# Kernel tuning notes

Hardware: AMD Instinct MI355X
Metric: run time of the kernel (lower is better)

## Reference

```python
import jax, jax.numpy as jnp
import numpy as np

N_NODES = 100000
N_EDGES = 1600000
D_IN = 128
D_HID = 128
N_CLASSES = 4
N_GRAPHS = 512


def setup_inputs() -> dict:
    key = jax.random.key(0)
    ks = jax.random.split(key, 10)
    x = jax.random.normal(ks[0], (N_NODES, D_IN), dtype=jnp.float32)
    edge_index = jax.random.randint(ks[1], (2, N_EDGES), 0, N_NODES, dtype=jnp.int64)
    batch = jnp.sort(jax.random.randint(ks[2], (N_NODES,), 0, N_GRAPHS, dtype=jnp.int64))
    s = 1.0 / np.sqrt(D_IN)
    W1l = jax.random.uniform(ks[3], (D_HID, D_IN), jnp.float32, -s, s)
    W1r = jax.random.uniform(ks[4], (D_HID, D_IN), jnp.float32, -s, s)
    b1 = jnp.zeros((D_HID,), jnp.float32)
    s2 = 1.0 / np.sqrt(D_HID)
    W2l = jax.random.uniform(ks[5], (D_HID, D_HID), jnp.float32, -s2, s2)
    W2r = jax.random.uniform(ks[6], (D_HID, D_HID), jnp.float32, -s2, s2)
    b2 = jnp.zeros((D_HID,), jnp.float32)
    Wlin = jax.random.uniform(ks[7], (N_CLASSES, D_HID), jnp.float32, -s2, s2)
    blin = jax.random.uniform(ks[8], (N_CLASSES,), jnp.float32, -s2, s2)
    return {"x": x, "edge_index": edge_index, "batch": batch,
            "W1l": W1l, "b1": b1, "W1r": W1r,
            "W2l": W2l, "b2": b2, "W2r": W2r,
            "Wlin": Wlin, "blin": blin}


def _sage_conv(x, src, dst, deg_inv, W_l, b, W_r):
    # mean-aggregate neighbor features (messages flow src -> dst)
    agg = jax.ops.segment_sum(x[src], dst, num_segments=N_NODES) * deg_inv
    return agg @ W_l.T + b + x @ W_r.T


def reference(x, edge_index, batch, W1l, b1, W1r, W2l, b2, W2r, Wlin, blin):
    src, dst = edge_index[0], edge_index[1]
    ones = jnp.ones((src.shape[0],), x.dtype)
    deg = jax.ops.segment_sum(ones, dst, num_segments=N_NODES)
    deg_inv = (1.0 / jnp.maximum(deg, 1.0))[:, None]

    h = jax.nn.relu(_sage_conv(x, src, dst, deg_inv, W1l, b1, W1r))
    h = jax.nn.relu(_sage_conv(h, src, dst, deg_inv, W2l, b2, W2r))

    # global mean pool over graphs
    gsum = jax.ops.segment_sum(h, batch, num_segments=N_GRAPHS)
    gcnt = jax.ops.segment_sum(jnp.ones((N_NODES,), h.dtype), batch, num_segments=N_GRAPHS)
    pooled = gsum / jnp.maximum(gcnt, 1.0)[:, None]

    # dropout is identity in eval mode
    return pooled @ Wlin.T + blin
```

## Files before the change

kernel.cpp:

```cpp
#include <hip/hip_runtime.h>
#include <hip/hip_bf16.h>


#define NN 100000
#define NE 1600000
#define DH 128
#define NG 512
#define CSTRIDE 48
#define NPREP 6250

#define SUBSH 8
#define SUBN  256
#define NSUB  391
#define CAP   4608
#define NSCAN 256
#define ESPS  6250

#define PSUM_SCALE  1048576.0f
#define PSUM_INV    (1.0f/1048576.0f)

typedef __hip_bfloat16 bf16;
typedef __bf16 bf16x8 __attribute__((ext_vector_type(8)));
typedef float  f32x4  __attribute__((ext_vector_type(4)));
typedef float  f32x2  __attribute__((ext_vector_type(2)));
typedef unsigned u32x2 __attribute__((ext_vector_type(2)));
typedef unsigned u32x4 __attribute__((ext_vector_type(4)));
typedef unsigned char u8;

__device__ __forceinline__ void bf8_to_f(uint4 q, float* w) {
    union { unsigned u; float f; } t;
    t.u = q.x << 16;          w[0] = t.f;
    t.u = q.x & 0xffff0000u;  w[1] = t.f;
    t.u = q.y << 16;          w[2] = t.f;
    t.u = q.y & 0xffff0000u;  w[3] = t.f;
    t.u = q.z << 16;          w[4] = t.f;
    t.u = q.z & 0xffff0000u;  w[5] = t.f;
    t.u = q.w << 16;          w[6] = t.f;
    t.u = q.w & 0xffff0000u;  w[7] = t.f;
}

__device__ __forceinline__ unsigned pack4_fp8(float a, float b, float c, float d) {
    int p = __builtin_amdgcn_cvt_pk_fp8_f32(a, b, 0, false);
    p = __builtin_amdgcn_cvt_pk_fp8_f32(c, d, p, true);
    return (unsigned)p;
}


__global__ __launch_bounds__(256) void k_prep(
    const int* __restrict__ ei, int* __restrict__ ccnt,
    const float* __restrict__ x, u8* __restrict__ fq,
    const float* __restrict__ w0, const float* __restrict__ w1,
    const float* __restrict__ w2, const float* __restrict__ w3,
    bf16* __restrict__ wb,
    const int* __restrict__ batch, int* __restrict__ cnt)
{
    const int bid = blockIdx.x, tid = threadIdx.x;

    if (bid < NSCAN) {
        __shared__ int c[NSUB];
        for (int i = tid; i < NSUB; i += 256) c[i] = 0;
        __syncthreads();
        const int e0 = bid * ESPS;
        for (int e = e0 + tid; e < e0 + ESPS; e += 256) {
            int d = __builtin_nontemporal_load(ei + NE + e);
            atomicAdd(&c[d >> SUBSH], 1);
        }
        __syncthreads();
        for (int i = tid; i < NSUB; i += 256) ccnt[i * NSCAN + bid] = c[i];
        return;
    }

    const int pb = bid - NSCAN;
    {
        int g = pb * 256 + tid;
        const f32x4* s = (const f32x4*)(x + (size_t)g * 8);
        f32x4 u0 = __builtin_nontemporal_load(s);
        f32x4 u1 = __builtin_nontemporal_load(s + 1);
        u32x2 v;
        v[0] = pack4_fp8(u0[0], u0[1], u0[2], u0[3]);
        v[1] = pack4_fp8(u1[0], u1[1], u1[2], u1[3]);
        __builtin_nontemporal_store(v, (u32x2*)(fq + (size_t)g * 8));
    }
    if (pb < 256) {
        int gid = pb * 256 + tid;
        int m = gid >> 14, i = gid & 16383;
        const float* src = (m == 0) ? w0 : (m == 1) ? w1 : (m == 2) ? w2 : w3;
        wb[gid] = __float2bfloat16(src[i]);
    } else if (pb < 258) {
        int g = (pb - 256) * 256 + tid;
        if (g < NG) {
            int lo0 = 0, hi0 = NN, lo1 = 0, hi1 = NN;
            while (lo0 < hi0) { int m = (lo0 + hi0) >> 1; if (batch[m] < g)     lo0 = m + 1; else hi0 = m; }
            while (lo1 < hi1) { int m = (lo1 + hi1) >> 1; if (batch[m] < g + 1) lo1 = m + 1; else hi1 = m; }
            cnt[g] = lo1 - lo0;
        }
    } else if (pb == 258) {
        if (tid < 8) {
            uint4 z = {0u, 0u, 0u, 0u};
            ((uint4*)(fq + (size_t)NN * DH))[tid] = z;
        }
    }
}


__global__ __launch_bounds__(256) void k_rowscan(
    const int* __restrict__ ccnt, int* __restrict__ bofs, int* __restrict__ tot)
{
    const int g = blockIdx.x, t = threadIdx.x;
    __shared__ int s[256];
    int v = ccnt[g * NSCAN + t];
    s[t] = v;
    __syncthreads();
    #pragma unroll
    for (int off = 1; off < 256; off <<= 1) {
        int tmp = (t >= off) ? s[t - off] : 0;
        __syncthreads();
        s[t] += tmp;
        __syncthreads();
    }
    bofs[g * NSCAN + t] = s[t] - v;
    if (t == 255) tot[g] = s[255];
}


__global__ __launch_bounds__(256) void k_scatter(
    const int* __restrict__ ei, const int* __restrict__ bofs,
    unsigned* __restrict__ pe)
{
    const int s = blockIdx.x, tid = threadIdx.x;
    __shared__ int rank[NSUB];
    for (int g = tid; g < NSUB; g += 256)
        rank[g] = g * CAP + bofs[g * NSCAN + s];
    __syncthreads();

    const int e0 = s * ESPS;
    for (int e = e0 + tid; e < e0 + ESPS; e += 256) {
        int d   = __builtin_nontemporal_load(ei + NE + e);
        int src = __builtin_nontemporal_load(ei + e);
        int g = d >> SUBSH;
        int pos = atomicAdd(&rank[g], 1);
        if (pos < (g + 1) * CAP)
            pe[pos] = ((unsigned)(d & (SUBN - 1)) << 17) | (unsigned)src;
    }
}


__global__ __launch_bounds__(256) void k_fill2(
    const unsigned* __restrict__ pe, const int* __restrict__ tot,
    int* __restrict__ deg, int* __restrict__ col)
{
    const int g = blockIdx.x, tid = threadIdx.x;
    __shared__ int degL[SUBN];
    degL[tid] = 0;
    __syncthreads();

    const int lo = g * CAP;
    const int n  = min(tot[g], CAP);
    const int nb = g << SUBSH;
    for (int e = lo + tid; e < lo + n; e += 256) {
        unsigned p = pe[e];
        int src = (int)(p & 0x1FFFFu);
        int dl  = (int)(p >> 17);
        int pos = atomicAdd(&degL[dl], 1);
        if (pos < CSTRIDE) col[(nb + dl) * CSTRIDE + pos] = src;
    }
    __syncthreads();

    int node = nb + tid;
    if (node < NN) deg[node] = degL[tid];
}


__global__ __launch_bounds__(256) void k_gather(
    const int* __restrict__ deg, const int* __restrict__ col,
    const u8* __restrict__ fq, bf16* __restrict__ agg)
{
    const int nid  = blockIdx.x * 4 + (threadIdx.x >> 6);
    const int lane = threadIdx.x & 63;
    const int qsub = lane >> 4;
    const int l4   = lane & 15;
    int dgr = __builtin_amdgcn_readfirstlane(deg[nid]);
    int dg = dgr > CSTRIDE ? CSTRIDE : dgr;
    int vidx = (lane < dg) ? col[nid * CSTRIDE + lane] : NN;

    f32x2 a0 = {0.f, 0.f}, a1 = {0.f, 0.f}, a2 = {0.f, 0.f}, a3 = {0.f, 0.f};
    f32x2 b0 = {0.f, 0.f}, b1 = {0.f, 0.f}, b2 = {0.f, 0.f}, b3 = {0.f, 0.f};
    const unsigned l8 = (unsigned)l4 * 8u;

    for (int e = 0; e < dg; e += 8) {
        int sA = __shfl(vidx, e + qsub, 64);
        int sB = __shfl(vidx, e + 4 + qsub, 64);
        uint2 qA = *(const uint2*)(fq + (((unsigned)sA << 7) + l8));
        uint2 qB = *(const uint2*)(fq + (((unsigned)sB << 7) + l8));
        a0 += __builtin_amdgcn_cvt_pk_f32_fp8((int)qA.x, false);
        a1 += __builtin_amdgcn_cvt_pk_f32_fp8((int)qA.x, true);
        a2 += __builtin_amdgcn_cvt_pk_f32_fp8((int)qA.y, false);
        a3 += __builtin_amdgcn_cvt_pk_f32_fp8((int)qA.y, true);
        b0 += __builtin_amdgcn_cvt_pk_f32_fp8((int)qB.x, false);
        b1 += __builtin_amdgcn_cvt_pk_f32_fp8((int)qB.x, true);
        b2 += __builtin_amdgcn_cvt_pk_f32_fp8((int)qB.y, false);
        b3 += __builtin_amdgcn_cvt_pk_f32_fp8((int)qB.y, true);
    }
    a0 += b0; a1 += b1; a2 += b2; a3 += b3;

    float a[8] = {a0[0], a0[1], a1[0], a1[1], a2[0], a2[1], a3[0], a3[1]};
    #pragma unroll
    for (int i = 0; i < 8; ++i) {
        a[i] += __shfl_xor(a[i], 16, 64);
        a[i] += __shfl_xor(a[i], 32, 64);
    }

    if (qsub == 0) {
        float di = 1.0f / fmaxf((float)dgr, 1.0f);
        union { bf16 b[8]; u32x4 u; } pk;
        #pragma unroll
        for (int i = 0; i < 8; ++i) pk.b[i] = __float2bfloat16(a[i] * di);
        __builtin_nontemporal_store(pk.u, (u32x4*)(agg + nid * DH + l4 * 8));
    }
}


#define WSTR 136

template <bool POOL>
__global__ __launch_bounds__(256, 4) void k_layer(
    const bf16* __restrict__ agg, const u8* __restrict__ xq,
    const bf16* __restrict__ Wlb, const bf16* __restrict__ Wrb,
    const float* __restrict__ bias,
    u8* __restrict__ outq, int* __restrict__ psum,
    const int* __restrict__ batch)
{
    __shared__ bf16 wl[128 * WSTR];
    __shared__ int  bb[128];

    const int tid  = threadIdx.x;
    const int wave = tid >> 6;
    const int lane = tid & 63;
    const int lm   = lane & 15;
    const int kg   = lane >> 4;
    const int base = blockIdx.x * 128;
    const int wbase = base + wave * 32;

    const int r0 = min(wbase + lm,      NN - 1);
    const int r1 = min(wbase + 16 + lm, NN - 1);

    if (POOL && tid < 128) bb[tid] = batch[min(base + tid, NN - 1)];

    {
        const int row = tid >> 1, half = tid & 1;
        const uint4* src = (const uint4*)(Wlb + row * DH + half * 64);
        uint4* dst = (uint4*)(wl + row * WSTR + half * 64);
        #pragma unroll
        for (int i = 0; i < 8; ++i) dst[i] = src[i];
    }
    __syncthreads();

    f32x4 acc[2][8];
    #pragma unroll
    for (int i = 0; i < 2; ++i)
        #pragma unroll
        for (int t = 0; t < 8; ++t)
            acc[i][t] = (f32x4){0.f, 0.f, 0.f, 0.f};

    #pragma unroll
    for (int kc = 0; kc < 4; ++kc) {
        const int ko = kc * 32 + kg * 8;
        bf16x8 a0 = *(const bf16x8*)(agg + r0 * DH + ko);
        bf16x8 a1 = *(const bf16x8*)(agg + r1 * DH + ko);
        #pragma unroll
        for (int t = 0; t < 8; ++t) {
            bf16x8 b = *(const bf16x8*)(wl + (t * 16 + lm) * WSTR + ko);
            acc[0][t] = __builtin_amdgcn_mfma_f32_16x16x32_bf16(a0, b, acc[0][t], 0, 0, 0);
            acc[1][t] = __builtin_amdgcn_mfma_f32_16x16x32_bf16(a1, b, acc[1][t], 0, 0, 0);
        }
    }
    __syncthreads();

    {
        const int row = tid >> 1, half = tid & 1;
        const uint4* src = (const uint4*)(Wrb + row * DH + half * 64);
        uint4* dst = (uint4*)(wl + row * WSTR + half * 64);
        #pragma unroll
        for (int i = 0; i < 8; ++i) dst[i] = src[i];
    }
    __syncthreads();

    #pragma unroll
    for (int kc = 0; kc < 4; ++kc) {
        const int ko = kc * 32 + kg * 8;
        bf16x8 a0, a1;
        uint2 q0 = *(const uint2*)(xq + (size_t)r0 * DH + ko);
        uint2 q1 = *(const uint2*)(xq + (size_t)r1 * DH + ko);
        f32x2 c0 = __builtin_amdgcn_cvt_pk_f32_fp8((int)q0.x, false);
        f32x2 c1 = __builtin_amdgcn_cvt_pk_f32_fp8((int)q0.x, true);
        f32x2 c2 = __builtin_amdgcn_cvt_pk_f32_fp8((int)q0.y, false);
        f32x2 c3 = __builtin_amdgcn_cvt_pk_f32_fp8((int)q0.y, true);
        a0[0] = (__bf16)c0[0]; a0[1] = (__bf16)c0[1];
        a0[2] = (__bf16)c1[0]; a0[3] = (__bf16)c1[1];
        a0[4] = (__bf16)c2[0]; a0[5] = (__bf16)c2[1];
        a0[6] = (__bf16)c3[0]; a0[7] = (__bf16)c3[1];
        c0 = __builtin_amdgcn_cvt_pk_f32_fp8((int)q1.x, false);
        c1 = __builtin_amdgcn_cvt_pk_f32_fp8((int)q1.x, true);
        c2 = __builtin_amdgcn_cvt_pk_f32_fp8((int)q1.y, false);
        c3 = __builtin_amdgcn_cvt_pk_f32_fp8((int)q1.y, true);
        a1[0] = (__bf16)c0[0]; a1[1] = (__bf16)c0[1];
        a1[2] = (__bf16)c1[0]; a1[3] = (__bf16)c1[1];
        a1[4] = (__bf16)c2[0]; a1[5] = (__bf16)c2[1];
        a1[6] = (__bf16)c3[0]; a1[7] = (__bf16)c3[1];
        #pragma unroll
        for (int t = 0; t < 8; ++t) {
            bf16x8 b = *(const bf16x8*)(wl + (t * 16 + lm) * WSTR + ko);
            acc[0][t] = __builtin_amdgcn_mfma_f32_16x16x32_bf16(a0, b, acc[0][t], 0, 0, 0);
            acc[1][t] = __builtin_amdgcn_mfma_f32_16x16x32_bf16(a1, b, acc[1][t], 0, 0, 0);
        }
    }
    __syncthreads();

    bf16* ob = wl;
    const int quad = lane >> 4;
    #pragma unroll
    for (int i = 0; i < 2; ++i) {
        #pragma unroll
        for (int r = 0; r < 4; ++r) {
            const int lr = wave * 32 + i * 16 + quad * 4 + r;
            const int n  = base + lr;
            #pragma unroll
            for (int t = 0; t < 8; ++t) {
                const int f = t * 16 + lm;
                float v = fmaxf(acc[i][t][r] + bias[f], 0.f);
                if (POOL && n >= NN) v = 0.f;
                ob[lr * DH + f] = __float2bfloat16(v);
            }
        }
    }
    __syncthreads();

    if (!POOL) {
        uint2* d = (uint2*)(outq + (size_t)base * DH);
        #pragma unroll
        for (int i = 0; i < 8; ++i) {
            const int idx = i * 256 + tid;
            const int n = base + (idx >> 4);
            if (n < NN) {
                uint4 s = ((const uint4*)ob)[idx];
                float w[8];
                bf8_to_f(s, w);
                uint2 o;
                o.x = pack4_fp8(w[0], w[1], w[2], w[3]);
                o.y = pack4_fp8(w[4], w[5], w[6], w[7]);
                d[idx] = o;
            }
        }
    } else {
        const int f = tid & 127, h = tid >> 7;
        float rs = 0.f;
        int cur = bb[h * 64];
        #pragma unroll 8
        for (int r = 0; r < 64; ++r) {
            const int row = h * 64 + r;
            float v = __bfloat162float(ob[row * DH + f]);
            int b = bb[row];
            if (b != cur) {
                atomicAdd(&psum[cur * DH + f], __float2int_rn(rs * PSUM_SCALE));
                rs = 0.f; cur = b;
            }
            rs += v;
        }
        atomicAdd(&psum[cur * DH + f], __float2int_rn(rs * PSUM_SCALE));
    }
}


__global__ __launch_bounds__(256) void k_final(
    const int* __restrict__ psum, const int* __restrict__ cnt,
    const float* __restrict__ Wlin, const float* __restrict__ blin,
    float* __restrict__ out)
{
    int gid = blockIdx.x * 256 + threadIdx.x;
    if (gid >= NG * 4) return;
    int gph = gid >> 2, c = gid & 3;
    const int* p = psum + gph * DH;
    const float* w = Wlin + c * DH;
    float s = 0.f;
    #pragma unroll 8
    for (int k = 0; k < DH; ++k)
        s += (float)p[k] * w[k];
    float inv = 1.0f / fmaxf((float)cnt[gph], 1.0f);
    out[gid] = s * PSUM_INV * inv + blin[c];
}

extern "C" void kernel_launch(void* const* d_in, const int* in_sizes, int n_in,
                              void* d_out, int out_size, void* d_ws, size_t ws_size,
                              hipStream_t stream) {
    const float* x     = (const float*)d_in[0];
    const int*   ei    = (const int*)d_in[1];
    const int*   batch = (const int*)d_in[2];
    const float* W1l   = (const float*)d_in[3];
    const float* b1    = (const float*)d_in[4];
    const float* W1r   = (const float*)d_in[5];
    const float* W2l   = (const float*)d_in[6];
    const float* b2    = (const float*)d_in[7];
    const float* W2r   = (const float*)d_in[8];
    const float* Wlin  = (const float*)d_in[9];
    const float* blin  = (const float*)d_in[10];
    float* out = (float*)d_out;

    char* base = (char*)d_ws;
    int*      deg  = (int*)(base + 64);
    int*      cnt  = (int*)(base + 400064);
    int*      psum = (int*)(base + 402112);
    bf16*     wb   = (bf16*)(base + 664256);
    int*      ccnt = (int*)(base + 795328);
    int*      bofs = (int*)(base + 1195712);
    int*      tot  = (int*)(base + 1596096);
    int*      col  = (int*)(base + 1597696);
    bf16*     agg  = (bf16*)(base + 20797696);
    u8*       fq   = (u8*)(base + 46397696);
    unsigned* pe   = (unsigned*)(base + 59200000);

    bf16* W1lb = wb;
    bf16* W1rb = wb + 16384;
    bf16* W2lb = wb + 32768;
    bf16* W2rb = wb + 49152;

    hipMemsetAsync(base + 402112, 0, 262144, stream);

    k_prep<<<NSCAN + NPREP, 256, 0, stream>>>(
        ei, ccnt, x, fq, W1l, W1r, W2l, W2r, wb, batch, cnt);
    k_rowscan<<<NSUB, 256, 0, stream>>>(ccnt, bofs, tot);
    k_scatter<<<NSCAN, 256, 0, stream>>>(ei, bofs, pe);
    k_fill2<<<NSUB, 256, 0, stream>>>(pe, tot, deg, col);

    k_gather<<<NN / 4, 256, 0, stream>>>(deg, col, fq, agg);
    k_layer<false><<<(NN + 127) / 128, 256, 0, stream>>>(agg, fq, W1lb, W1rb, b1,
                                                         fq, nullptr, nullptr);

    k_gather<<<NN / 4, 256, 0, stream>>>(deg, col, fq, agg);
    k_layer<true><<<(NN + 127) / 128, 256, 0, stream>>>(agg, fq, W2lb, W2rb, b2,
                                                        nullptr, psum, batch);

    k_final<<<8, 256, 0, stream>>>(psum, cnt, Wlin, blin, out);
}
```

Baseline: 298.6 us.

## Make gather kernel persistent with two nodes per wave and prefetched adjacency

The gather kernel moves from one block per four nodes to a fixed grid of persistent blocks. Each wavefront now handles two nodes per iteration and walks the node range with a grid stride. The next pair's degree and column indices are prefetched while the current pair is accumulated. The inner loop is unrolled to issue eight independent fp8 row loads per step, which raises memory-level parallelism and cuts launch and scheduling overhead. In exchange, the loop runs to the larger of the two degrees, so some lanes do padded work, and register pressure goes up.

Result: faster. 288.8 us (-3.3%).

```diff
diff --git a/kernel.cpp b/kernel.cpp
--- a/kernel.cpp
+++ b/kernel.cpp
@@ -15,6 +15,7 @@
 #define CAP   4608
 #define NSCAN 256
 #define ESPS  6250
+#define GBLK  2048
 
 #define PSUM_SCALE  1048576.0f
 #define PSUM_INV    (1.0f/1048576.0f)
@@ -175,47 +176,120 @@
     const int* __restrict__ deg, const int* __restrict__ col,
     const u8* __restrict__ fq, bf16* __restrict__ agg)
 {
-    const int nid  = blockIdx.x * 4 + (threadIdx.x >> 6);
     const int lane = threadIdx.x & 63;
     const int qsub = lane >> 4;
     const int l4   = lane & 15;
-    int dgr = __builtin_amdgcn_readfirstlane(deg[nid]);
-    int dg = dgr > CSTRIDE ? CSTRIDE : dgr;
-    int vidx = (lane < dg) ? col[nid * CSTRIDE + lane] : NN;
-
-    f32x2 a0 = {0.f, 0.f}, a1 = {0.f, 0.f}, a2 = {0.f, 0.f}, a3 = {0.f, 0.f};
-    f32x2 b0 = {0.f, 0.f}, b1 = {0.f, 0.f}, b2 = {0.f, 0.f}, b3 = {0.f, 0.f};
     const unsigned l8 = (unsigned)l4 * 8u;
-
-    for (int e = 0; e < dg; e += 8) {
-        int sA = __shfl(vidx, e + qsub, 64);
-        int sB = __shfl(vidx, e + 4 + qsub, 64);
-        uint2 qA = *(const uint2*)(fq + (((unsigned)sA << 7) + l8));
-        uint2 qB = *(const uint2*)(fq + (((unsigned)sB << 7) + l8));
-        a0 += __builtin_amdgcn_cvt_pk_f32_fp8((int)qA.x, false);
-        a1 += __builtin_amdgcn_cvt_pk_f32_fp8((int)qA.x, true);
-        a2 += __builtin_amdgcn_cvt_pk_f32_fp8((int)qA.y, false);
-        a3 += __builtin_amdgcn_cvt_pk_f32_fp8((int)qA.y, true);
-        b0 += __builtin_amdgcn_cvt_pk_f32_fp8((int)qB.x, false);
-        b1 += __builtin_amdgcn_cvt_pk_f32_fp8((int)qB.x, true);
-        b2 += __builtin_amdgcn_cvt_pk_f32_fp8((int)qB.y, false);
-        b3 += __builtin_amdgcn_cvt_pk_f32_fp8((int)qB.y, true);
-    }
-    a0 += b0; a1 += b1; a2 += b2; a3 += b3;
-
-    float a[8] = {a0[0], a0[1], a1[0], a1[1], a2[0], a2[1], a3[0], a3[1]};
-    #pragma unroll
-    for (int i = 0; i < 8; ++i) {
-        a[i] += __shfl_xor(a[i], 16, 64);
-        a[i] += __shfl_xor(a[i], 32, 64);
-    }
-
-    if (qsub == 0) {
-        float di = 1.0f / fmaxf((float)dgr, 1.0f);
-        union { bf16 b[8]; u32x4 u; } pk;
-        #pragma unroll
-        for (int i = 0; i < 8; ++i) pk.b[i] = __float2bfloat16(a[i] * di);
-        __builtin_nontemporal_store(pk.u, (u32x4*)(agg + nid * DH + l4 * 8));
+    const int wid  = blockIdx.x * 4 + (threadIdx.x >> 6);
+    const int NSTR = GBLK * 4 * 2;
+
+    int nA = wid * 2;
+
+    int dgrA = deg[nA];
+    int dgrB = deg[nA + 1];
+    int vrawA = (lane < CSTRIDE) ? col[nA * CSTRIDE + lane] : 0;
+    int vrawB = (lane < CSTRIDE) ? col[(nA + 1) * CSTRIDE + lane] : 0;
+
+    while (true) {
+        const int nN = nA + NSTR;
+        const bool more = nN < NN;
+        int dgrAN = 0, dgrBN = 0, vrawAN = 0, vrawBN = 0;
+        if (more) {
+            dgrAN = deg[nN];
+            dgrBN = deg[nN + 1];
+            vrawAN = (lane < CSTRIDE) ? col[nN * CSTRIDE + lane] : 0;
+            vrawBN = (lane < CSTRIDE) ? col[(nN + 1) * CSTRIDE + lane] : 0;
+        }
+
+        const int dgsA = __builtin_amdgcn_readfirstlane(dgrA);
+        const int dgsB = __builtin_amdgcn_readfirstlane(dgrB);
+        const int dgA = dgsA > CSTRIDE ? CSTRIDE : dgsA;
+        const int dgB = dgsB > CSTRIDE ? CSTRIDE : dgsB;
+        const int dgM = dgA > dgB ? dgA : dgB;
+        int vidxA = (lane < dgA) ? vrawA : NN;
+        int vidxB = (lane < dgB) ? vrawB : NN;
+
+        f32x2 aA0 = {0.f, 0.f}, aA1 = {0.f, 0.f}, aA2 = {0.f, 0.f}, aA3 = {0.f, 0.f};
+        f32x2 aB0 = {0.f, 0.f}, aB1 = {0.f, 0.f}, aB2 = {0.f, 0.f}, aB3 = {0.f, 0.f};
+
+        for (int e = 0; e < dgM; e += 16) {
+            int sA0 = __shfl(vidxA, e + qsub,      64);
+            int sA1 = __shfl(vidxA, e + 4 + qsub,  64);
+            int sA2 = __shfl(vidxA, e + 8 + qsub,  64);
+            int sA3 = __shfl(vidxA, e + 12 + qsub, 64);
+            int sB0 = __shfl(vidxB, e + qsub,      64);
+            int sB1 = __shfl(vidxB, e + 4 + qsub,  64);
+            int sB2 = __shfl(vidxB, e + 8 + qsub,  64);
+            int sB3 = __shfl(vidxB, e + 12 + qsub, 64);
+            uint2 qA0 = *(const uint2*)(fq + (((unsigned)sA0 << 7) + l8));
+            uint2 qA1 = *(const uint2*)(fq + (((unsigned)sA1 << 7) + l8));
+            uint2 qA2 = *(const uint2*)(fq + (((unsigned)sA2 << 7) + l8));
+            uint2 qA3 = *(const uint2*)(fq + (((unsigned)sA3 << 7) + l8));
+            uint2 qB0 = *(const uint2*)(fq + (((unsigned)sB0 << 7) + l8));
+            uint2 qB1 = *(const uint2*)(fq + (((unsigned)sB1 << 7) + l8));
+            uint2 qB2 = *(const uint2*)(fq + (((unsigned)sB2 << 7) + l8));
+            uint2 qB3 = *(const uint2*)(fq + (((unsigned)sB3 << 7) + l8));
+            aA0 += __builtin_amdgcn_cvt_pk_f32_fp8((int)qA0.x, false);
+            aA1 += __builtin_amdgcn_cvt_pk_f32_fp8((int)qA0.x, true);
+            aA2 += __builtin_amdgcn_cvt_pk_f32_fp8((int)qA0.y, false);
+            aA3 += __builtin_amdgcn_cvt_pk_f32_fp8((int)qA0.y, true);
+            aA0 += __builtin_amdgcn_cvt_pk_f32_fp8((int)qA1.x, false);
+            aA1 += __builtin_amdgcn_cvt_pk_f32_fp8((int)qA1.x, true);
+            aA2 += __builtin_amdgcn_cvt_pk_f32_fp8((int)qA1.y, false);
+            aA3 += __builtin_amdgcn_cvt_pk_f32_fp8((int)qA1.y, true);
+            aA0 += __builtin_amdgcn_cvt_pk_f32_fp8((int)qA2.x, false);
+            aA1 += __builtin_amdgcn_cvt_pk_f32_fp8((int)qA2.x, true);
+            aA2 += __builtin_amdgcn_cvt_pk_f32_fp8((int)qA2.y, false);
+            aA3 += __builtin_amdgcn_cvt_pk_f32_fp8((int)qA2.y, true);
+            aA0 += __builtin_amdgcn_cvt_pk_f32_fp8((int)qA3.x, false);
+            aA1 += __builtin_amdgcn_cvt_pk_f32_fp8((int)qA3.x, true);
+            aA2 += __builtin_amdgcn_cvt_pk_f32_fp8((int)qA3.y, false);
+            aA3 += __builtin_amdgcn_cvt_pk_f32_fp8((int)qA3.y, true);
+            aB0 += __builtin_amdgcn_cvt_pk_f32_fp8((int)qB0.x, false);
+            aB1 += __builtin_amdgcn_cvt_pk_f32_fp8((int)qB0.x, true);
+            aB2 += __builtin_amdgcn_cvt_pk_f32_fp8((int)qB0.y, false);
+            aB3 += __builtin_amdgcn_cvt_pk_f32_fp8((int)qB0.y, true);
+            aB0 += __builtin_amdgcn_cvt_pk_f32_fp8((int)qB1.x, false);
+            aB1 += __builtin_amdgcn_cvt_pk_f32_fp8((int)qB1.x, true);
+            aB2 += __builtin_amdgcn_cvt_pk_f32_fp8((int)qB1.y, false);
+            aB3 += __builtin_amdgcn_cvt_pk_f32_fp8((int)qB1.y, true);
+            aB0 += __builtin_amdgcn_cvt_pk_f32_fp8((int)qB2.x, false);
+            aB1 += __builtin_amdgcn_cvt_pk_f32_fp8((int)qB2.x, true);
+            aB2 += __builtin_amdgcn_cvt_pk_f32_fp8((int)qB2.y, false);
+            aB3 += __builtin_amdgcn_cvt_pk_f32_fp8((int)qB2.y, true);
+            aB0 += __builtin_amdgcn_cvt_pk_f32_fp8((int)qB3.x, false);
+            aB1 += __builtin_amdgcn_cvt_pk_f32_fp8((int)qB3.x, true);
+            aB2 += __builtin_amdgcn_cvt_pk_f32_fp8((int)qB3.y, false);
+            aB3 += __builtin_amdgcn_cvt_pk_f32_fp8((int)qB3.y, true);
+        }
+
+        float rA[8] = {aA0[0], aA0[1], aA1[0], aA1[1], aA2[0], aA2[1], aA3[0], aA3[1]};
+        float rB[8] = {aB0[0], aB0[1], aB1[0], aB1[1], aB2[0], aB2[1], aB3[0], aB3[1]};
+        #pragma unroll
+        for (int i = 0; i < 8; ++i) {
+            rA[i] += __shfl_xor(rA[i], 16, 64);
+            rB[i] += __shfl_xor(rB[i], 16, 64);
+            rA[i] += __shfl_xor(rA[i], 32, 64);
+            rB[i] += __shfl_xor(rB[i], 32, 64);
+        }
+
+        if (qsub == 0) {
+            float di = 1.0f / fmaxf((float)dgsA, 1.0f);
+            union { bf16 b[8]; u32x4 u; } pk;
+            #pragma unroll
+            for (int i = 0; i < 8; ++i) pk.b[i] = __float2bfloat16(rA[i] * di);
+            __builtin_nontemporal_store(pk.u, (u32x4*)(agg + nA * DH + l4 * 8));
+        } else if (qsub == 1) {
+            float di = 1.0f / fmaxf((float)dgsB, 1.0f);
+            union { bf16 b[8]; u32x4 u; } pk;
+            #pragma unroll
+            for (int i = 0; i < 8; ++i) pk.b[i] = __float2bfloat16(rB[i] * di);
+            __builtin_nontemporal_store(pk.u, (u32x4*)(agg + (nA + 1) * DH + l4 * 8));
+        }
+
+        if (!more) break;
+        nA = nN;
+        dgrA = dgrAN; dgrB = dgrBN; vrawA = vrawAN; vrawB = vrawBN;
     }
 }
 
@@ -431,11 +505,11 @@
     k_scatter<<<NSCAN, 256, 0, stream>>>(ei, bofs, pe);
     k_fill2<<<NSUB, 256, 0, stream>>>(pe, tot, deg, col);
 
-    k_gather<<<NN / 4, 256, 0, stream>>>(deg, col, fq, agg);
+    k_gather<<<GBLK, 256, 0, stream>>>(deg, col, fq, agg);
     k_layer<false><<<(NN + 127) / 128, 256, 0, stream>>>(agg, fq, W1lb, W1rb, b1,
                                                          fq, nullptr, nullptr);
 
-    k_gather<<<NN / 4, 256, 0, stream>>>(deg, col, fq, agg);
+    k_gather<<<GBLK, 256, 0, stream>>>(deg, col, fq, agg);
     k_layer<true><<<(NN + 127) / 128, 256, 0, stream>>>(agg, fq, W2lb, W2rb, b2,
                                                         nullptr, psum, batch);
 
```
